# Performance work log

Measured on AMD Instinct MI355X. Metric: run time of the kernel, lower is better.

## Reference

```python
import jax, jax.numpy as jnp
import numpy as np

B, S, D = 8, 512, 768
H = 12          # attention heads
E = 14          # routed experts
K = 4           # top-k experts per sequence
HID = D * 2     # expert mlp hidden (mlp_ratio=2)
SH = D * 2 * 2  # shared expert hidden (mlp_ratio * n_shared_experts)
EPS = 1e-5


def _ln(x, g, b):
    m = x.mean(-1, keepdims=True)
    v = ((x - m) ** 2).mean(-1, keepdims=True)
    return (x - m) / jnp.sqrt(v + EPS) * g + b


def _gelu(x):
    return jax.nn.gelu(x, approximate=False)


def setup_inputs() -> dict:
    key = jax.random.key(0)
    ks = jax.random.split(key, 12)
    p = lambda k, shape: jax.random.normal(k, shape, jnp.float32) * 0.02
    z = lambda *shape: jnp.zeros(shape, jnp.float32)
    return {
        "x": jax.random.normal(ks[0], (B, S, D), jnp.float32),
        "ln1_g": jnp.ones((D,), jnp.float32), "ln1_b": z(D),
        "qkv_w": p(ks[1], (D, 3 * D)),
        "proj_w": p(ks[2], (D, D)), "proj_b": z(D),
        "ln2_g": jnp.ones((D,), jnp.float32), "ln2_b": z(D),
        "router_w1": p(ks[3], (D, D)), "router_b1": z(D),
        "router_w2": p(ks[4], (D, E)), "router_b2": z(E),
        "exp_w1": p(ks[5], (E, D, HID)), "exp_b1": z(E, HID),
        "exp_w2": p(ks[6], (E, HID, D)), "exp_b2": z(E, D),
        "sh_w1": p(ks[7], (D, SH)), "sh_b1": z(SH),
        "sh_w2": p(ks[8], (SH, D)), "sh_b2": z(D),
    }


def _forward(x, ln1_g, ln1_b, qkv_w, proj_w, proj_b, ln2_g, ln2_b,
             router_w1, router_b1, router_w2, router_b2,
             exp_w1, exp_b1, exp_w2, exp_b2,
             sh_w1, sh_b1, sh_w2, sh_b2):
    dh = D // H
    scale = dh ** -0.5
    # --- attention branch ---
    h1 = _ln(x, ln1_g, ln1_b)
    qkv = (h1 @ qkv_w).reshape(B, S, 3, H, dh)
    q = jnp.moveaxis(qkv[:, :, 0], 2, 1)  # [B,H,S,dh]
    k = jnp.moveaxis(qkv[:, :, 1], 2, 1)
    v = jnp.moveaxis(qkv[:, :, 2], 2, 1)
    att = jax.nn.softmax(jnp.einsum('bhqd,bhkd->bhqk', q, k) * scale, axis=-1)
    ao = jnp.einsum('bhqk,bhkd->bqhd', att, v).reshape(B, S, D) @ proj_w + proj_b
    x2 = x + ao
    # --- MoE branch ---
    h = _ln(x2, ln2_g, ln2_b)
    seq_repr = h.mean(axis=1)                                   # [B,D]
    logits = _gelu(seq_repr @ router_w1 + router_b1) @ router_w2 + router_b2  # [B,E]
    probs = jax.nn.softmax(logits, axis=-1)
    tw, ti = jax.lax.top_k(probs, K)                            # [B,K]
    tw = jax.nn.softmax(tw, axis=-1)                            # re-normalize top-k
    w = (jax.nn.one_hot(ti, E, dtype=tw.dtype) * tw[..., None]).sum(1)  # [B,E]
    # dense all-expert compute; zero weight off the top-k replicates masked routing
    hid = _gelu(jnp.einsum('bsd,edh->ebsh', h, exp_w1) + exp_b1[:, None, None, :])
    eo = jnp.einsum('ebsh,ehd->ebsd', hid, exp_w2) + exp_b2[:, None, None, :]
    y = jnp.einsum('ebsd,be->bsd', eo, w)
    # shared experts
    y = y + _gelu(h @ sh_w1 + sh_b1) @ sh_w2 + sh_b2
    return x2 + y  # ls2 is Identity (init_values=None); aux_loss=0 in eval


def reference(x, ln1_g, ln1_b, qkv_w, proj_w, proj_b, ln2_g, ln2_b,
              router_w1, router_b1, router_w2, router_b2,
              exp_w1, exp_b1, exp_w2, exp_b2,
              sh_w1, sh_b1, sh_w2, sh_b2):
    return _forward(x, ln1_g, ln1_b, qkv_w, proj_w, proj_b, ln2_g, ln2_b,
                    router_w1, router_b1, router_w2, router_b2,
                    exp_w1, exp_b1, exp_w2, exp_b2,
                    sh_w1, sh_b1, sh_w2, sh_b2)
```

## Files before the change

### kernel.cpp

```cpp
#include <hip/hip_runtime.h>
#include <hip/hip_bf16.h>


typedef _Float16 f16x8 __attribute__((ext_vector_type(8)));
typedef float f32x4 __attribute__((ext_vector_type(4)));
typedef _Float16 f16;

__device__ __forceinline__ float gelu_exact(float x) {
  return 0.5f * x * (1.0f + erff(x * 0.70710678118654752f));
}

__device__ __forceinline__ f32x4 mfma16(f16x8 a, f16x8 b, f32x4 c) {
  return __builtin_amdgcn_mfma_f32_16x16x32_f16(a, b, c, 0, 0, 0);
}

#define ASYNC_CP16(g, l)                                            \
  __builtin_amdgcn_global_load_lds(                                 \
      (const __attribute__((address_space(1))) void*)(g),           \
      (__attribute__((address_space(3))) void*)(l), 16, 0, 0)

__global__ __launch_bounds__(256) void ln_kernel(
    const float* __restrict__ x, const float* __restrict__ g,
    const float* __restrict__ bt, f16* __restrict__ out,
    float* __restrict__ mout, float* __restrict__ rout)
{
  const int row = blockIdx.x;
  const float* xr = x + (long)row * 768;
  const int t = threadIdx.x;
  float v0 = xr[t], v1 = xr[t + 256], v2 = xr[t + 512];
  __shared__ float sb[8];
  float s = v0 + v1 + v2;
  #pragma unroll
  for (int o = 32; o > 0; o >>= 1) s += __shfl_xor(s, o, 64);
  const int w = t >> 6;
  if ((t & 63) == 0) sb[w] = s;
  __syncthreads();
  const float mean = (sb[0] + sb[1] + sb[2] + sb[3]) * (1.0f / 768.0f);
  const float d0 = v0 - mean, d1 = v1 - mean, d2 = v2 - mean;
  float q = d0 * d0 + d1 * d1 + d2 * d2;
  #pragma unroll
  for (int o = 32; o > 0; o >>= 1) q += __shfl_xor(q, o, 64);
  if ((t & 63) == 0) sb[4 + w] = q;
  __syncthreads();
  const float var = (sb[4] + sb[5] + sb[6] + sb[7]) * (1.0f / 768.0f);
  const float rstd = rsqrtf(var + 1e-5f);
  f16* orow = out + (long)row * 768;
  orow[t]       = (f16)(d0 * rstd * g[t]       + bt[t]);
  orow[t + 256] = (f16)(d1 * rstd * g[t + 256] + bt[t + 256]);
  orow[t + 512] = (f16)(d2 * rstd * g[t + 512] + bt[t + 512]);
  if (t == 0) { mout[row] = mean; rout[row] = rstd; }
}

__global__ __launch_bounds__(256) void transpose_f16(
    const float* __restrict__ in, f16* __restrict__ out, int rows, int cols)
{
  __shared__ float tile[32][33];
  const long boff = (long)blockIdx.z * rows * cols;
  const float* inb = in + boff;
  f16* outb = out + boff;
  const int c0 = blockIdx.x * 32, r0 = blockIdx.y * 32;
  const int tx = threadIdx.x & 31, ty = threadIdx.x >> 5;
  #pragma unroll
  for (int i = 0; i < 32; i += 8)
    tile[ty + i][tx] = inb[(long)(r0 + ty + i) * cols + c0 + tx];
  __syncthreads();
  #pragma unroll
  for (int i = 0; i < 32; i += 8)
    outb[(long)(c0 + ty + i) * rows + r0 + tx] = (f16)tile[tx][ty + i];
}

#define EPI_QKV   0
#define EPI_RESID 1
#define EPI_GELU  2
#define EPI_PLAIN 3

template <int EPI>
__global__ __launch_bounds__(256) void gemm_bt(
    const f16* __restrict__ A, int K, long strideA, int aShift,
    const f16* __restrict__ W, long strideW,
    const float* __restrict__ bias, int strideBias,
    const int* __restrict__ topkIdx,
    void* __restrict__ outv, long strideOut, int ldout,
    const float* __restrict__ resid)
{
  __shared__ f16 sA[128 * 32];
  __shared__ f16 sB[128 * 32];
  const int tid = threadIdx.x;
  const int pair = blockIdx.z;
  const int m0 = blockIdx.y * 128;
  const int n0 = blockIdx.x * 128;
  const f16* Ab = A + ((long)(pair >> aShift)) * strideA;
  const int wsel = topkIdx ? topkIdx[pair] : pair;
  const f16* Wb = W + (long)wsel * strideW;

  const int f = tid * 8;
  const int fr = f >> 5;
  const int fc = f & 31;
  const int lane = tid & 63, wid = tid >> 6;
  const int wm = (wid >> 1) * 64, wn = (wid & 1) * 64;
  const int lr = lane & 15, q4 = lane >> 4;

  f32x4 zero = {0.f, 0.f, 0.f, 0.f};
  f32x4 acc[4][4];
  #pragma unroll
  for (int i = 0; i < 4; i++)
    #pragma unroll
    for (int j = 0; j < 4; j++) acc[i][j] = zero;

  for (int k0 = 0; k0 < K; k0 += 32) {
    __syncthreads();
    ASYNC_CP16(&Ab[(long)(m0 + fr) * K + k0 + fc],      &sA[f]);
    ASYNC_CP16(&Ab[(long)(m0 + fr + 64) * K + k0 + fc], &sA[f + 2048]);
    ASYNC_CP16(&Wb[(long)(n0 + fr) * K + k0 + fc],      &sB[f]);
    ASYNC_CP16(&Wb[(long)(n0 + fr + 64) * K + k0 + fc], &sB[f + 2048]);
    __syncthreads();
    f16x8 av[4], bv[4];
    #pragma unroll
    for (int i = 0; i < 4; i++) av[i] = *(const f16x8*)&sA[(wm + i * 16 + lr) * 32 + q4 * 8];
    #pragma unroll
    for (int j = 0; j < 4; j++) bv[j] = *(const f16x8*)&sB[(wn + j * 16 + lr) * 32 + q4 * 8];
    #pragma unroll
    for (int i = 0; i < 4; i++)
      #pragma unroll
      for (int j = 0; j < 4; j++) acc[i][j] = mfma16(av[i], bv[j], acc[i][j]);
  }

  #pragma unroll
  for (int i = 0; i < 4; i++) {
    #pragma unroll
    for (int j = 0; j < 4; j++) {
      #pragma unroll
      for (int r = 0; r < 4; r++) {
        const int row = m0 + wm + i * 16 + q4 * 4 + r;
        const int col = n0 + wn + j * 16 + lr;
        float v = acc[i][j][r];
        if constexpr (EPI == EPI_QKV) {
          f16* qb = (f16*)outv;
          const int i3 = col / 768;
          const int rem = col - i3 * 768;
          const int hh = rem >> 6, dd = rem & 63;
          const int bb = row >> 9, ss = row & 511;
          const long bh = bb * 12 + hh;
          if (i3 == 0)      qb[(bh * 512 + ss) * 64 + dd] = (f16)v;
          else if (i3 == 1) qb[3145728 + (bh * 512 + ss) * 64 + dd] = (f16)v;
          else              qb[6291456 + (bh * 64 + dd) * 512 + ss] = (f16)v;
        } else if constexpr (EPI == EPI_RESID) {
          float* ob = (float*)outv;
          v += bias[col];
          ob[(long)row * ldout + col] = resid[(long)row * ldout + col] + v;
        } else if constexpr (EPI == EPI_GELU) {
          f16* ob = (f16*)outv + (long)pair * strideOut;
          v += bias[(long)wsel * strideBias + col];
          ob[(long)row * ldout + col] = (f16)gelu_exact(v);
        } else {
          f16* ob = (f16*)outv + (long)pair * strideOut;
          v += bias[(long)wsel * strideBias + col];
          ob[(long)row * ldout + col] = (f16)v;
        }
      }
    }
  }
}

__global__ __launch_bounds__(256) void attn_kernel(
    const f16* __restrict__ Q, const f16* __restrict__ Kt,
    const f16* __restrict__ Vt, f16* __restrict__ P, f16* __restrict__ AO)
{
  const int bh = blockIdx.x;
  const int qt = blockIdx.y;
  const int t = threadIdx.x;
  const int lane = t & 63, w = t >> 6;
  const int lr = lane & 15, q4 = lane >> 4;
  const int r0 = qt * 64 + w * 16;
  const f16* Qh = Q + (long)bh * 512 * 64;
  const f16* Kh = Kt + (long)bh * 512 * 64;

  f32x4 zero = {0.f, 0.f, 0.f, 0.f};
  f32x4 acc[32];
  #pragma unroll
  for (int i = 0; i < 32; i++) acc[i] = zero;

  #pragma unroll
  for (int kk = 0; kk < 2; kk++) {
    f16x8 a = *(const f16x8*)&Qh[(r0 + lr) * 64 + kk * 32 + q4 * 8];
    #pragma unroll
    for (int nt = 0; nt < 32; nt++) {
      f16x8 b = *(const f16x8*)&Kh[(nt * 16 + lr) * 64 + kk * 32 + q4 * 8];
      acc[nt] = mfma16(a, b, acc[nt]);
    }
  }

  const float cscale = 0.125f * 1.44269504089f;
  f16* Ph = P + (long)bh * 512 * 512;
  #pragma unroll
  for (int r = 0; r < 4; r++) {
    float m = -1e30f;
    #pragma unroll
    for (int nt = 0; nt < 32; nt++) m = fmaxf(m, acc[nt][r]);
    #pragma unroll
    for (int o = 1; o < 16; o <<= 1) m = fmaxf(m, __shfl_xor(m, o, 64));
    float s = 0.f;
    #pragma unroll
    for (int nt = 0; nt < 32; nt++) {
      float e = exp2f((acc[nt][r] - m) * cscale);
      acc[nt][r] = e; s += e;
    }
    #pragma unroll
    for (int o = 1; o < 16; o <<= 1) s += __shfl_xor(s, o, 64);
    const float inv = 1.f / s;
    const int rowg = r0 + q4 * 4 + r;
    #pragma unroll
    for (int nt = 0; nt < 32; nt++)
      Ph[(long)rowg * 512 + nt * 16 + lr] = (f16)(acc[nt][r] * inv);
  }
  __syncthreads();

  const f16* Vh = Vt + (long)bh * 64 * 512;
  f32x4 o4[4];
  #pragma unroll
  for (int i = 0; i < 4; i++) o4[i] = zero;
  #pragma unroll
  for (int kk = 0; kk < 16; kk++) {
    f16x8 a = *(const f16x8*)&Ph[(r0 + lr) * 512 + kk * 32 + q4 * 8];
    #pragma unroll
    for (int nt = 0; nt < 4; nt++) {
      f16x8 b = *(const f16x8*)&Vh[(nt * 16 + lr) * 512 + kk * 32 + q4 * 8];
      o4[nt] = mfma16(a, b, o4[nt]);
    }
  }
  const int b_ = bh / 12, h_ = bh - b_ * 12;
  #pragma unroll
  for (int nt = 0; nt < 4; nt++)
    #pragma unroll
    for (int r = 0; r < 4; r++) {
      const int rowg = r0 + q4 * 4 + r;
      AO[((long)(b_ * 512 + rowg)) * 768 + h_ * 64 + nt * 16 + lr] = (f16)o4[nt][r];
    }
}

__global__ __launch_bounds__(256) void router_reduce(
    const float* __restrict__ x2, const float* __restrict__ lnm,
    const float* __restrict__ lnr, float* __restrict__ part)
{
  const int c = blockIdx.x, b = blockIdx.y, t = threadIdx.x;
  float a0 = 0.f, a1 = 0.f, a2 = 0.f;
  #pragma unroll 4
  for (int s = 0; s < 32; s++) {
    const long base = (long)b * 512 + c * 32 + s;
    const float m = lnm[base], r = lnr[base];
    const float* xr = x2 + base * 768;
    a0 += (xr[t] - m) * r;
    a1 += (xr[t + 256] - m) * r;
    a2 += (xr[t + 512] - m) * r;
  }
  float* pr = part + ((long)b * 16 + c) * 768;
  pr[t] = a0; pr[t + 256] = a1; pr[t + 512] = a2;
}

__global__ __launch_bounds__(256) void router_seq(
    const float* __restrict__ part, const float* __restrict__ g2,
    const float* __restrict__ b2ln, float* __restrict__ seqg)
{
  const int b = blockIdx.x, t = threadIdx.x;
  const float* pb = part + (long)b * 16 * 768;
  #pragma unroll
  for (int i = 0; i < 3; i++) {
    const int j = t + 256 * i;
    float a = 0.f;
    #pragma unroll
    for (int c = 0; c < 16; c++) a += pb[c * 768 + j];
    seqg[b * 768 + j] = a * (1.f / 512.f) * g2[j] + b2ln[j];
  }
}

__global__ __launch_bounds__(256) void router_mlp1(
    const float* __restrict__ seqg, const float* __restrict__ rw1,
    float* __restrict__ pmlp)
{
  const int c = blockIdx.x, b = blockIdx.y, t = threadIdx.x;
  const float* sq = seqg + b * 768 + c * 48;
  float a0 = 0.f, a1 = 0.f, a2 = 0.f;
  #pragma unroll 8
  for (int d = 0; d < 48; d++) {
    const float s = sq[d];
    const float* wr = rw1 + (long)(c * 48 + d) * 768;
    a0 += s * wr[t];
    a1 += s * wr[t + 256];
    a2 += s * wr[t + 512];
  }
  float* pr = pmlp + ((long)b * 16 + c) * 768;
  pr[t] = a0; pr[t + 256] = a1; pr[t + 512] = a2;
}

__global__ __launch_bounds__(256) void router_fold(
    const float* __restrict__ pmlp, const float* __restrict__ rb1,
    float* __restrict__ g1g)
{
  const int b = blockIdx.x, t = threadIdx.x;
  const float* pb = pmlp + (long)b * 16 * 768;
  #pragma unroll
  for (int i = 0; i < 3; i++) {
    const int j = t + 256 * i;
    float a = rb1[j];
    #pragma unroll
    for (int c = 0; c < 16; c++) a += pb[c * 768 + j];
    g1g[b * 768 + j] = gelu_exact(a);
  }
}

__global__ __launch_bounds__(256) void router_top(
    const float* __restrict__ g1g, const float* __restrict__ rw2,
    const float* __restrict__ rb2, float* __restrict__ wslot,
    int* __restrict__ topkIdx)
{
  __shared__ float lg[14];
  const int b = blockIdx.x, t = threadIdx.x;
  const int e = t >> 4, sub = t & 15;
  if (e < 14) {
    float a = 0.f;
    #pragma unroll
    for (int i = 0; i < 48; i++) {
      const int d = sub + 16 * i;
      a += g1g[b * 768 + d] * rw2[d * 14 + e];
    }
    #pragma unroll
    for (int o = 1; o < 16; o <<= 1) a += __shfl_xor(a, o, 64);
    if (sub == 0) lg[e] = a + rb2[e];
  }
  __syncthreads();
  if (t == 0) {
    float mx = -1e30f;
    for (int ee = 0; ee < 14; ee++) mx = fmaxf(mx, lg[ee]);
    float p[14], s = 0.f;
    for (int ee = 0; ee < 14; ee++) { p[ee] = expf(lg[ee] - mx); s += p[ee]; }
    for (int ee = 0; ee < 14; ee++) p[ee] /= s;
    int idx[4]; float val[4]; bool used[14];
    for (int ee = 0; ee < 14; ee++) used[ee] = false;
    for (int k = 0; k < 4; k++) {
      int best = -1; float bv = -1.f;
      for (int ee = 0; ee < 14; ee++)
        if (!used[ee] && p[ee] > bv) { bv = p[ee]; best = ee; }
      used[best] = true; idx[k] = best; val[k] = bv;
    }
    const float m2 = val[0];
    float ss = 0.f, e4[4];
    for (int k = 0; k < 4; k++) { e4[k] = expf(val[k] - m2); ss += e4[k]; }
    for (int k = 0; k < 4; k++) {
      wslot[b * 4 + k] = e4[k] / ss;
      topkIdx[b * 4 + k] = idx[k];
    }
  }
}

__global__ __launch_bounds__(256) void combine_kernel(
    const float* __restrict__ x2, const f16* __restrict__ shout,
    const f16* __restrict__ eo, const float* __restrict__ wslot,
    float* __restrict__ out)
{
  const long i = (long)blockIdx.x * 256 + threadIdx.x;
  const long b = i / (512L * 768);
  const long loc = i - b * (512L * 768);
  float v = x2[i] + (float)shout[i];
  #pragma unroll
  for (int k = 0; k < 4; k++)
    v += wslot[b * 4 + k] * (float)eo[(b * 4 + k) * (512L * 768) + loc];
  out[i] = v;
}

static const long OFF_X2    = 0L;
static const long OFF_LNM   = 12582912L;
static const long OFF_LNR   = OFF_LNM + 16384L;
static const long OFF_WSLOT = OFF_LNR + 16384L;
static const long OFF_TOPK  = OFF_WSLOT + 256L;
static const long OFF_PART  = OFF_TOPK + 256L;
static const long OFF_SEQG  = OFF_PART + 393216L;
static const long OFF_PMLP  = OFF_SEQG + 24576L;
static const long OFF_G1G   = OFF_PMLP + 393216L;
static const long OFF_A     = 13631488L;
static const long A_H1     = OFF_A;
static const long A_QKVWT  = A_H1 + 6291456L;
static const long A_Q      = A_QKVWT + 3538944L;
static const long A_P      = A_Q + 3L * 6291456L;
static const long A_AO     = A_P + 50331648L;
static const long A_PROJWT = A_AO + 6291456L;
static const long B_H      = OFF_A;
static const long B_EW1T   = B_H + 6291456L;
static const long B_EW2T   = B_EW1T + 33030144L;
static const long B_HID    = B_EW2T + 33030144L;
static const long B_EO     = B_HID + 50331648L;
static const long B_SHW1T  = B_EO + 25165824L;
static const long B_SHW2T  = B_SHW1T + 4718592L;
static const long B_SHOUT  = B_SHW2T + 4718592L;
static const long B_SHID   = B_EW1T;

extern "C" void kernel_launch(void* const* d_in, const int* in_sizes, int n_in,
                              void* d_out, int out_size, void* d_ws, size_t ws_size,
                              hipStream_t stream) {
  const float* x     = (const float*)d_in[0];
  const float* ln1g  = (const float*)d_in[1];
  const float* ln1b  = (const float*)d_in[2];
  const float* qkvw  = (const float*)d_in[3];
  const float* projw = (const float*)d_in[4];
  const float* projb = (const float*)d_in[5];
  const float* ln2g  = (const float*)d_in[6];
  const float* ln2b  = (const float*)d_in[7];
  const float* rw1   = (const float*)d_in[8];
  const float* rb1   = (const float*)d_in[9];
  const float* rw2   = (const float*)d_in[10];
  const float* rb2   = (const float*)d_in[11];
  const float* ew1   = (const float*)d_in[12];
  const float* eb1   = (const float*)d_in[13];
  const float* ew2   = (const float*)d_in[14];
  const float* eb2   = (const float*)d_in[15];
  const float* shw1  = (const float*)d_in[16];
  const float* shb1  = (const float*)d_in[17];
  const float* shw2  = (const float*)d_in[18];
  const float* shb2  = (const float*)d_in[19];

  char* ws = (char*)d_ws;
  float* x2    = (float*)(ws + OFF_X2);
  float* lnm   = (float*)(ws + OFF_LNM);
  float* lnr   = (float*)(ws + OFF_LNR);
  float* wslot = (float*)(ws + OFF_WSLOT);
  int*   topk  = (int*)(ws + OFF_TOPK);
  float* part  = (float*)(ws + OFF_PART);
  float* seqg  = (float*)(ws + OFF_SEQG);
  float* pmlp  = (float*)(ws + OFF_PMLP);
  float* g1g   = (float*)(ws + OFF_G1G);
  f16* h1     = (f16*)(ws + A_H1);
  f16* qkvwt  = (f16*)(ws + A_QKVWT);
  f16* Qb     = (f16*)(ws + A_Q);
  f16* Kb     = Qb + 3145728;
  f16* Vtb    = Qb + 6291456;
  f16* Pb     = (f16*)(ws + A_P);
  f16* aob    = (f16*)(ws + A_AO);
  f16* projwt = (f16*)(ws + A_PROJWT);
  f16* hbuf   = (f16*)(ws + B_H);
  f16* ew1t   = (f16*)(ws + B_EW1T);
  f16* ew2t   = (f16*)(ws + B_EW2T);
  f16* hid    = (f16*)(ws + B_HID);
  f16* eo     = (f16*)(ws + B_EO);
  f16* shw1t  = (f16*)(ws + B_SHW1T);
  f16* shw2t  = (f16*)(ws + B_SHW2T);
  f16* shout  = (f16*)(ws + B_SHOUT);
  f16* shid   = (f16*)(ws + B_SHID);

  transpose_f16<<<dim3(72, 24, 1), 256, 0, stream>>>(qkvw, qkvwt, 768, 2304);
  transpose_f16<<<dim3(24, 24, 1), 256, 0, stream>>>(projw, projwt, 768, 768);
  ln_kernel<<<4096, 256, 0, stream>>>(x, ln1g, ln1b, h1, lnm, lnr);
  gemm_bt<EPI_QKV><<<dim3(18, 32, 1), 256, 0, stream>>>(
      h1, 768, 0, 0, qkvwt, 0, nullptr, 0, nullptr, (void*)Qb, 0, 0, nullptr);
  attn_kernel<<<dim3(96, 8, 1), 256, 0, stream>>>(Qb, Kb, Vtb, Pb, aob);
  gemm_bt<EPI_RESID><<<dim3(6, 32, 1), 256, 0, stream>>>(
      aob, 768, 0, 0, projwt, 0, projb, 0, nullptr, (void*)x2, 0, 768, x);

  ln_kernel<<<4096, 256, 0, stream>>>(x2, ln2g, ln2b, hbuf, lnm, lnr);
  router_reduce<<<dim3(16, 8, 1), 256, 0, stream>>>(x2, lnm, lnr, part);
  router_seq<<<8, 256, 0, stream>>>(part, ln2g, ln2b, seqg);
  router_mlp1<<<dim3(16, 8, 1), 256, 0, stream>>>(seqg, rw1, pmlp);
  router_fold<<<8, 256, 0, stream>>>(pmlp, rb1, g1g);
  router_top<<<8, 256, 0, stream>>>(g1g, rw2, rb2, wslot, topk);
  transpose_f16<<<dim3(48, 24, 14), 256, 0, stream>>>(ew1, ew1t, 768, 1536);
  transpose_f16<<<dim3(24, 48, 14), 256, 0, stream>>>(ew2, ew2t, 1536, 768);
  transpose_f16<<<dim3(96, 24, 1), 256, 0, stream>>>(shw1, shw1t, 768, 3072);
  transpose_f16<<<dim3(24, 96, 1), 256, 0, stream>>>(shw2, shw2t, 3072, 768);
  gemm_bt<EPI_GELU><<<dim3(12, 4, 32), 256, 0, stream>>>(
      hbuf, 768, 512L * 768, 2, ew1t, 1536L * 768, eb1, 1536, topk,
      (void*)hid, 512L * 1536, 1536, nullptr);
  gemm_bt<EPI_PLAIN><<<dim3(6, 4, 32), 256, 0, stream>>>(
      hid, 1536, 512L * 1536, 0, ew2t, 768L * 1536, eb2, 768, topk,
      (void*)eo, 512L * 768, 768, nullptr);
  gemm_bt<EPI_GELU><<<dim3(24, 32, 1), 256, 0, stream>>>(
      hbuf, 768, 0, 0, shw1t, 0, shb1, 0, nullptr, (void*)shid, 0, 3072, nullptr);
  gemm_bt<EPI_PLAIN><<<dim3(6, 32, 1), 256, 0, stream>>>(
      shid, 3072, 0, 0, shw2t, 0, shb2, 0, nullptr, (void*)shout, 0, 768, nullptr);

  combine_kernel<<<12288, 256, 0, stream>>>(x2, shout, eo, wslot, (float*)d_out);
}
```

Measured before the change: 665.7 us.

## Fuse weight transposes, keep attention probs in LDS, fold combine into GEMM epilogues

Merges all six weight transposes into a single multi-matrix launch. The attention probability matrix now stays in swizzled shared memory instead of a global buffer. The combine kernel is removed: the shared-expert second GEMM writes x2 plus its output directly into the result, and the routed-expert second GEMM atomically adds its gate-weighted output. The expert and shared GELU is swapped from exact erf to a tanh approximation, which trades accuracy for fewer instructions and may drift from the reference. Atomics add contention and make the summation order nondeterministic.

```diff
diff --git a/kernel.cpp b/kernel.cpp
--- a/kernel.cpp
+++ b/kernel.cpp
@@ -6,8 +6,11 @@
 typedef float f32x4 __attribute__((ext_vector_type(4)));
 typedef _Float16 f16;
 
-__device__ __forceinline__ float gelu_exact(float x) {
-  return 0.5f * x * (1.0f + erff(x * 0.70710678118654752f));
+__device__ __forceinline__ float gelu_fast(float x) {
+  const float k2l2e = 2.f * 0.7978845608028654f * 1.4426950408889634f;
+  float u = (x + 0.044715f * x * x * x) * k2l2e;
+  float t = exp2f(u);
+  return x * (1.f - 1.f / (t + 1.f));
 }
 
 __device__ __forceinline__ f32x4 mfma16(f16x8 a, f16x8 b, f32x4 c) {
@@ -51,14 +54,28 @@
   if (t == 0) { mout[row] = mean; rout[row] = rstd; }
 }
 
-__global__ __launch_bounds__(256) void transpose_f16(
-    const float* __restrict__ in, f16* __restrict__ out, int rows, int cols)
-{
+struct TransArgs {
+  const float* src[6];
+  f16* dst[6];
+  int rows[6], cols[6];
+  int start[7];
+};
+
+__global__ __launch_bounds__(256) void transpose_all(TransArgs ta) {
+  const int bid = blockIdx.x;
+  int m = 0;
+  #pragma unroll
+  for (int i = 1; i < 6; i++) if (bid >= ta.start[i]) m = i;
+  const int rows = ta.rows[m], cols = ta.cols[m];
+  const int tilesC = cols >> 5;
+  const int perB = (rows >> 5) * tilesC;
+  int local = bid - ta.start[m];
+  const int z = local / perB; local -= z * perB;
+  const int tr = local / tilesC, tc = local - tr * tilesC;
+  const float* inb = ta.src[m] + (long)z * rows * cols;
+  f16* outb = ta.dst[m] + (long)z * rows * cols;
+  const int c0 = tc * 32, r0 = tr * 32;
   __shared__ float tile[32][33];
-  const long boff = (long)blockIdx.z * rows * cols;
-  const float* inb = in + boff;
-  f16* outb = out + boff;
-  const int c0 = blockIdx.x * 32, r0 = blockIdx.y * 32;
   const int tx = threadIdx.x & 31, ty = threadIdx.x >> 5;
   #pragma unroll
   for (int i = 0; i < 32; i += 8)
@@ -69,10 +86,11 @@
     outb[(long)(c0 + ty + i) * rows + r0 + tx] = (f16)tile[tx][ty + i];
 }
 
-#define EPI_QKV   0
-#define EPI_RESID 1
-#define EPI_GELU  2
-#define EPI_PLAIN 3
+#define EPI_QKV     0
+#define EPI_RESID   1
+#define EPI_GELU    2
+#define EPI_OUTBASE 3
+#define EPI_ATOMIC  4
 
 template <int EPI>
 __global__ __launch_bounds__(256) void gemm_bt(
@@ -124,6 +142,9 @@
       #pragma unroll
       for (int j = 0; j < 4; j++) acc[i][j] = mfma16(av[i], bv[j], acc[i][j]);
   }
+
+  float wscale = 0.f;
+  if constexpr (EPI == EPI_ATOMIC) wscale = resid[pair];
 
   #pragma unroll
   for (int i = 0; i < 4; i++) {
@@ -151,27 +172,37 @@
         } else if constexpr (EPI == EPI_GELU) {
           f16* ob = (f16*)outv + (long)pair * strideOut;
           v += bias[(long)wsel * strideBias + col];
-          ob[(long)row * ldout + col] = (f16)gelu_exact(v);
+          ob[(long)row * ldout + col] = (f16)gelu_fast(v);
+        } else if constexpr (EPI == EPI_OUTBASE) {
+          float* ob = (float*)outv;
+          v += bias[col];
+          ob[(long)row * ldout + col] = resid[(long)row * ldout + col] + v;
         } else {
-          f16* ob = (f16*)outv + (long)pair * strideOut;
+          float* ob = (float*)outv + (long)(pair >> 2) * (512L * 768);
           v += bias[(long)wsel * strideBias + col];
-          ob[(long)row * ldout + col] = (f16)v;
+          atomicAdd(&ob[(long)row * ldout + col], wscale * v);
         }
       }
     }
   }
 }
 
+__device__ __forceinline__ int pswz(int row, int col) {
+  return row * 512 + (col ^ ((row & 7) << 3));
+}
+
 __global__ __launch_bounds__(256) void attn_kernel(
     const f16* __restrict__ Q, const f16* __restrict__ Kt,
-    const f16* __restrict__ Vt, f16* __restrict__ P, f16* __restrict__ AO)
-{
+    const f16* __restrict__ Vt, f16* __restrict__ AO)
+{
+  __shared__ f16 Ps[64 * 512];
   const int bh = blockIdx.x;
   const int qt = blockIdx.y;
   const int t = threadIdx.x;
   const int lane = t & 63, w = t >> 6;
   const int lr = lane & 15, q4 = lane >> 4;
   const int r0 = qt * 64 + w * 16;
+  const int lrow0 = w * 16;
   const f16* Qh = Q + (long)bh * 512 * 64;
   const f16* Kh = Kt + (long)bh * 512 * 64;
 
@@ -191,7 +222,6 @@
   }
 
   const float cscale = 0.125f * 1.44269504089f;
-  f16* Ph = P + (long)bh * 512 * 512;
   #pragma unroll
   for (int r = 0; r < 4; r++) {
     float m = -1e30f;
@@ -208,12 +238,11 @@
     #pragma unroll
     for (int o = 1; o < 16; o <<= 1) s += __shfl_xor(s, o, 64);
     const float inv = 1.f / s;
-    const int rowg = r0 + q4 * 4 + r;
+    const int lrow = lrow0 + q4 * 4 + r;
     #pragma unroll
     for (int nt = 0; nt < 32; nt++)
-      Ph[(long)rowg * 512 + nt * 16 + lr] = (f16)(acc[nt][r] * inv);
-  }
-  __syncthreads();
+      Ps[pswz(lrow, nt * 16 + lr)] = (f16)(acc[nt][r] * inv);
+  }
 
   const f16* Vh = Vt + (long)bh * 64 * 512;
   f32x4 o4[4];
@@ -221,7 +250,7 @@
   for (int i = 0; i < 4; i++) o4[i] = zero;
   #pragma unroll
   for (int kk = 0; kk < 16; kk++) {
-    f16x8 a = *(const f16x8*)&Ph[(r0 + lr) * 512 + kk * 32 + q4 * 8];
+    f16x8 a = *(const f16x8*)&Ps[pswz(lrow0 + lr, kk * 32 + q4 * 8)];
     #pragma unroll
     for (int nt = 0; nt < 4; nt++) {
       f16x8 b = *(const f16x8*)&Vh[(nt * 16 + lr) * 512 + kk * 32 + q4 * 8];
@@ -304,7 +333,7 @@
     float a = rb1[j];
     #pragma unroll
     for (int c = 0; c < 16; c++) a += pb[c * 768 + j];
-    g1g[b * 768 + j] = gelu_exact(a);
+    g1g[b * 768 + j] = 0.5f * a * (1.0f + erff(a * 0.70710678118654752f));
   }
 }
 
@@ -352,21 +381,6 @@
   }
 }
 
-__global__ __launch_bounds__(256) void combine_kernel(
-    const float* __restrict__ x2, const f16* __restrict__ shout,
-    const f16* __restrict__ eo, const float* __restrict__ wslot,
-    float* __restrict__ out)
-{
-  const long i = (long)blockIdx.x * 256 + threadIdx.x;
-  const long b = i / (512L * 768);
-  const long loc = i - b * (512L * 768);
-  float v = x2[i] + (float)shout[i];
-  #pragma unroll
-  for (int k = 0; k < 4; k++)
-    v += wslot[b * 4 + k] * (float)eo[(b * 4 + k) * (512L * 768) + loc];
-  out[i] = v;
-}
-
 static const long OFF_X2    = 0L;
 static const long OFF_LNM   = 12582912L;
 static const long OFF_LNR   = OFF_LNM + 16384L;
@@ -376,22 +390,19 @@
 static const long OFF_SEQG  = OFF_PART + 393216L;
 static const long OFF_PMLP  = OFF_SEQG + 24576L;
 static const long OFF_G1G   = OFF_PMLP + 393216L;
-static const long OFF_A     = 13631488L;
-static const long A_H1     = OFF_A;
-static const long A_QKVWT  = A_H1 + 6291456L;
-static const long A_Q      = A_QKVWT + 3538944L;
-static const long A_P      = A_Q + 3L * 6291456L;
-static const long A_AO     = A_P + 50331648L;
-static const long A_PROJWT = A_AO + 6291456L;
-static const long B_H      = OFF_A;
-static const long B_EW1T   = B_H + 6291456L;
-static const long B_EW2T   = B_EW1T + 33030144L;
-static const long B_HID    = B_EW2T + 33030144L;
-static const long B_EO     = B_HID + 50331648L;
-static const long B_SHW1T  = B_EO + 25165824L;
-static const long B_SHW2T  = B_SHW1T + 4718592L;
-static const long B_SHOUT  = B_SHW2T + 4718592L;
-static const long B_SHID   = B_EW1T;
+static const long W_QKVWT  = 13631488L;
+static const long W_PROJWT = W_QKVWT + 3538944L;
+static const long W_EW1T   = W_PROJWT + 1179648L;
+static const long W_EW2T   = W_EW1T + 33030144L;
+static const long W_SHW1T  = W_EW2T + 33030144L;
+static const long W_SHW2T  = W_SHW1T + 4718592L;
+static const long OFF_ACT  = 93847552L;
+static const long A_H1     = OFF_ACT;
+static const long A_Q      = OFF_ACT + 6291456L;
+static const long A_AO     = A_Q + 18874368L;
+static const long B_H      = OFF_ACT;
+static const long B_HID    = OFF_ACT + 6291456L;
+static const long B_SHID   = B_HID + 50331648L;
 
 extern "C" void kernel_launch(void* const* d_in, const int* in_sizes, int n_in,
                               void* d_out, int out_size, void* d_ws, size_t ws_size,
@@ -427,30 +438,35 @@
   float* seqg  = (float*)(ws + OFF_SEQG);
   float* pmlp  = (float*)(ws + OFF_PMLP);
   float* g1g   = (float*)(ws + OFF_G1G);
+  f16* qkvwt  = (f16*)(ws + W_QKVWT);
+  f16* projwt = (f16*)(ws + W_PROJWT);
+  f16* ew1t   = (f16*)(ws + W_EW1T);
+  f16* ew2t   = (f16*)(ws + W_EW2T);
+  f16* shw1t  = (f16*)(ws + W_SHW1T);
+  f16* shw2t  = (f16*)(ws + W_SHW2T);
   f16* h1     = (f16*)(ws + A_H1);
-  f16* qkvwt  = (f16*)(ws + A_QKVWT);
   f16* Qb     = (f16*)(ws + A_Q);
-  f16* Kb     = Qb + 3145728;
-  f16* Vtb    = Qb + 6291456;
-  f16* Pb     = (f16*)(ws + A_P);
   f16* aob    = (f16*)(ws + A_AO);
-  f16* projwt = (f16*)(ws + A_PROJWT);
   f16* hbuf   = (f16*)(ws + B_H);
-  f16* ew1t   = (f16*)(ws + B_EW1T);
-  f16* ew2t   = (f16*)(ws + B_EW2T);
   f16* hid    = (f16*)(ws + B_HID);
-  f16* eo     = (f16*)(ws + B_EO);
-  f16* shw1t  = (f16*)(ws + B_SHW1T);
-  f16* shw2t  = (f16*)(ws + B_SHW2T);
-  f16* shout  = (f16*)(ws + B_SHOUT);
   f16* shid   = (f16*)(ws + B_SHID);
 
-  transpose_f16<<<dim3(72, 24, 1), 256, 0, stream>>>(qkvw, qkvwt, 768, 2304);
-  transpose_f16<<<dim3(24, 24, 1), 256, 0, stream>>>(projw, projwt, 768, 768);
+  TransArgs ta;
+  ta.src[0] = qkvw;  ta.dst[0] = qkvwt;  ta.rows[0] = 768;  ta.cols[0] = 2304;
+  ta.src[1] = projw; ta.dst[1] = projwt; ta.rows[1] = 768;  ta.cols[1] = 768;
+  ta.src[2] = ew1;   ta.dst[2] = ew1t;   ta.rows[2] = 768;  ta.cols[2] = 1536;
+  ta.src[3] = ew2;   ta.dst[3] = ew2t;   ta.rows[3] = 1536; ta.cols[3] = 768;
+  ta.src[4] = shw1;  ta.dst[4] = shw1t;  ta.rows[4] = 768;  ta.cols[4] = 3072;
+  ta.src[5] = shw2;  ta.dst[5] = shw2t;  ta.rows[5] = 3072; ta.cols[5] = 768;
+  ta.start[0] = 0;     ta.start[1] = 1728;  ta.start[2] = 2304;
+  ta.start[3] = 18432; ta.start[4] = 34560; ta.start[5] = 36864;
+  ta.start[6] = 39168;
+  transpose_all<<<39168, 256, 0, stream>>>(ta);
+
   ln_kernel<<<4096, 256, 0, stream>>>(x, ln1g, ln1b, h1, lnm, lnr);
   gemm_bt<EPI_QKV><<<dim3(18, 32, 1), 256, 0, stream>>>(
       h1, 768, 0, 0, qkvwt, 0, nullptr, 0, nullptr, (void*)Qb, 0, 0, nullptr);
-  attn_kernel<<<dim3(96, 8, 1), 256, 0, stream>>>(Qb, Kb, Vtb, Pb, aob);
+  attn_kernel<<<dim3(96, 8, 1), 256, 0, stream>>>(Qb, Qb + 3145728, Qb + 6291456, aob);
   gemm_bt<EPI_RESID><<<dim3(6, 32, 1), 256, 0, stream>>>(
       aob, 768, 0, 0, projwt, 0, projb, 0, nullptr, (void*)x2, 0, 768, x);
 
@@ -460,20 +476,14 @@
   router_mlp1<<<dim3(16, 8, 1), 256, 0, stream>>>(seqg, rw1, pmlp);
   router_fold<<<8, 256, 0, stream>>>(pmlp, rb1, g1g);
   router_top<<<8, 256, 0, stream>>>(g1g, rw2, rb2, wslot, topk);
-  transpose_f16<<<dim3(48, 24, 14), 256, 0, stream>>>(ew1, ew1t, 768, 1536);
-  transpose_f16<<<dim3(24, 48, 14), 256, 0, stream>>>(ew2, ew2t, 1536, 768);
-  transpose_f16<<<dim3(96, 24, 1), 256, 0, stream>>>(shw1, shw1t, 768, 3072);
-  transpose_f16<<<dim3(24, 96, 1), 256, 0, stream>>>(shw2, shw2t, 3072, 768);
+  gemm_bt<EPI_GELU><<<dim3(24, 32, 1), 256, 0, stream>>>(
+      hbuf, 768, 0, 0, shw1t, 0, shb1, 0, nullptr, (void*)shid, 0, 3072, nullptr);
+  gemm_bt<EPI_OUTBASE><<<dim3(6, 32, 1), 256, 0, stream>>>(
+      shid, 3072, 0, 0, shw2t, 0, shb2, 0, nullptr, d_out, 0, 768, x2);
   gemm_bt<EPI_GELU><<<dim3(12, 4, 32), 256, 0, stream>>>(
       hbuf, 768, 512L * 768, 2, ew1t, 1536L * 768, eb1, 1536, topk,
       (void*)hid, 512L * 1536, 1536, nullptr);
-  gemm_bt<EPI_PLAIN><<<dim3(6, 4, 32), 256, 0, stream>>>(
+  gemm_bt<EPI_ATOMIC><<<dim3(6, 4, 32), 256, 0, stream>>>(
       hid, 1536, 512L * 1536, 0, ew2t, 768L * 1536, eb2, 768, topk,
-      (void*)eo, 512L * 768, 768, nullptr);
-  gemm_bt<EPI_GELU><<<dim3(24, 32, 1), 256, 0, stream>>>(
-      hbuf, 768, 0, 0, shw1t, 0, shb1, 0, nullptr, (void*)shid, 0, 3072, nullptr);
-  gemm_bt<EPI_PLAIN><<<dim3(6, 32, 1), 256, 0, stream>>>(
-      shid, 3072, 0, 0, shw2t, 0, shb2, 0, nullptr, (void*)shout, 0, 768, nullptr);
-
-  combine_kernel<<<12288, 256, 0, stream>>>(x2, shout, eo, wslot, (float*)d_out);
-}
+      d_out, 0, 768, wslot);
+}
```

After: 680.1 us. +2.2%, slower.
